# Performance work log

Hardware: AMD Instinct MI355X
Metric: run time of the kernel (lower is better)

The kernel has to match this reference:

```python
import jax, jax.numpy as jnp
import numpy as np

Q_MAX = 127.0  # int8 symmetric quant range


def setup_inputs() -> dict:
    key = jax.random.key(0)
    kx, kw, ks = jax.random.split(key, 3)
    M, K, N = 16384, 4096, 4096
    x = jax.random.normal(kx, (M, K), dtype=jnp.float32)
    # int8 weight values in [-127, 127]
    weight = jax.random.randint(kw, (N, K), -127, 128, dtype=jnp.int32).astype(jnp.int8)
    # per-output-row dequant scale, small positive values as a real quantizer would produce
    weight_scale = jax.random.uniform(ks, (N, 1), dtype=jnp.float32, minval=1e-3, maxval=1e-2)
    return {"x": x, "weight": weight, "weight_scale": weight_scale}


def reference(x, weight, weight_scale):
    # --- per-token dynamic activation quantization (get_hip_quant(per_Token)) ---
    amax = jnp.max(jnp.abs(x), axis=-1, keepdims=True)            # [M,1]
    x_scale = amax / Q_MAX                                        # [M,1]
    x_q = jnp.clip(jnp.round(x / jnp.maximum(x_scale, 1e-8)), -Q_MAX, Q_MAX)  # int8 values, kept fp32
    # --- gemm_a8w8: int8xint8 GEMM with fused dequant (row scale_a * col scale_b) ---
    acc = jnp.einsum('mk,nk->mn', x_q, weight.astype(jnp.float32),
                     preferred_element_type=jnp.float32)          # [M,N] int accumulation in fp32
    y = acc * x_scale * weight_scale.T                            # fused dequant scales
    return y  # fp32 stand-in for otype=bf16 output
```

## Files before the change

### kernel.cpp

```cpp
#include <hip/hip_runtime.h>
#include <stdint.h>

#define M_DIM 16384
#define N_DIM 4096
#define K_DIM 4096

#define BM 256
#define BN 256
#define BK 128
#define NT (K_DIM / BK)

typedef int i32x4 __attribute__((ext_vector_type(4)));

__device__ __forceinline__ void async16(const uint8_t* g, uint8_t* l) {
    __builtin_amdgcn_global_load_lds(
        (const __attribute__((address_space(1))) void*)g,
        (__attribute__((address_space(3))) void*)l,
        16, 0, 0);
}

__global__ __launch_bounds__(256) void pack_w_kernel(const int* __restrict__ w32,
                                                     uint32_t* __restrict__ w8,
                                                     int n4) {
    int i = blockIdx.x * 256 + threadIdx.x;
    if (i < n4) {
        const int4 v = reinterpret_cast<const int4*>(w32)[i];
        uint32_t p = (uint32_t)(v.x & 255) | ((uint32_t)(v.y & 255) << 8) |
                     ((uint32_t)(v.z & 255) << 16) | ((uint32_t)(v.w & 255) << 24);
        w8[i] = p;
    }
}

__global__ __launch_bounds__(256) void quant_kernel(const float* __restrict__ x,
                                                    uint32_t* __restrict__ xq,
                                                    float* __restrict__ xscale) {
    const int m = blockIdx.x;
    const int t = threadIdx.x;
    const float4* row = reinterpret_cast<const float4*>(x + (size_t)m * K_DIM);
    float4 v[4];
    float amax = 0.0f;
#pragma unroll
    for (int i = 0; i < 4; ++i) {
        v[i] = row[t + i * 256];
        amax = fmaxf(amax, fmaxf(fmaxf(fabsf(v[i].x), fabsf(v[i].y)),
                                 fmaxf(fabsf(v[i].z), fabsf(v[i].w))));
    }
#pragma unroll
    for (int off = 32; off > 0; off >>= 1) amax = fmaxf(amax, __shfl_xor(amax, off));
    __shared__ float smax[4];
    if ((t & 63) == 0) smax[t >> 6] = amax;
    __syncthreads();
    amax = fmaxf(fmaxf(smax[0], smax[1]), fmaxf(smax[2], smax[3]));
    const float scale = amax / 127.0f;
    const float s = fmaxf(scale, 1e-8f);
    if (t == 0) xscale[m] = scale;
    uint32_t* orow = xq + (size_t)m * (K_DIM / 4);
#pragma unroll
    for (int i = 0; i < 4; ++i) {
        int q0 = __float2int_rn(v[i].x / s);
        int q1 = __float2int_rn(v[i].y / s);
        int q2 = __float2int_rn(v[i].z / s);
        int q3 = __float2int_rn(v[i].w / s);
        q0 = max(-127, min(127, q0));
        q1 = max(-127, min(127, q1));
        q2 = max(-127, min(127, q2));
        q3 = max(-127, min(127, q3));
        uint32_t p = (uint32_t)(q0 & 255) | ((uint32_t)(q1 & 255) << 8) |
                     ((uint32_t)(q2 & 255) << 16) | ((uint32_t)(q3 & 255) << 24);
        orow[t + i * 256] = p;
    }
}

__global__ __launch_bounds__(512, 2) void gemm_kernel(
    const uint8_t* __restrict__ Aq, const float* __restrict__ ascale,
    const uint8_t* __restrict__ Bq, const float* __restrict__ wscale,
    float* __restrict__ out) {
    __shared__ uint8_t lds[4 * BM * BK];
    uint8_t* ldsA0 = lds;
    uint8_t* ldsA1 = lds + BM * BK;
    uint8_t* ldsB0 = lds + 2 * BM * BK;
    uint8_t* ldsB1 = lds + 3 * BM * BK;

    const int tid = threadIdx.x;
    const int lane = tid & 63;
    const int w = tid >> 6;
    const int wr = w >> 2;
    const int wc = w & 3;
    const int lr = lane & 15;
    const int lg = lane >> 4;

    const int bid = blockIdx.x;
    const int swz = (bid & 7) * (1024 / 8) + (bid >> 3);
    const size_t row0 = (size_t)(swz >> 4) * BM;
    const size_t col0 = (size_t)(swz & 15) * BN;
    const uint8_t* Ab = Aq + row0 * K_DIM;
    const uint8_t* Bb = Bq + col0 * K_DIM;

    i32x4 acc[8][4];
#pragma unroll
    for (int i = 0; i < 8; ++i)
#pragma unroll
        for (int j = 0; j < 4; ++j) acc[i][j] = (i32x4){0, 0, 0, 0};

#define STAGE_P(BASE, DST, KT)                                                   \
    do {                                                                         \
        _Pragma("unroll") for (int it_ = 0; it_ < 4; ++it_) {                    \
            const int idx_ = it_ * 512 + tid;                                    \
            const int m_ = idx_ >> 3, p_ = idx_ & 7;                             \
            async16((BASE) + (size_t)m_ * K_DIM + (KT) * BK +                    \
                        ((p_ ^ (m_ & 7)) << 4),                                  \
                    (DST) + (it_ * 512 + w * 64) * 16);                          \
        }                                                                        \
    } while (0)

#define READ_K(BUFA, BUFB, KK, F)                                                \
    do {                                                                         \
        _Pragma("unroll") for (int q_ = 0; q_ < 8; ++q_) {                       \
            const int r_ = wr * 128 + q_ * 16 + lr;                              \
            const int u_ = (KK) * 4 + lg;                                        \
            afk[F][q_] = *reinterpret_cast<const i32x4*>(                        \
                (BUFA) + r_ * BK + ((u_ ^ (r_ & 7)) << 4));                      \
        }                                                                        \
        _Pragma("unroll") for (int p_ = 0; p_ < 4; ++p_) {                       \
            const int r_ = wc * 64 + p_ * 16 + lr;                               \
            const int u_ = (KK) * 4 + lg;                                        \
            bfk[F][p_] = *reinterpret_cast<const i32x4*>(                        \
                (BUFB) + r_ * BK + ((u_ ^ (r_ & 7)) << 4));                      \
        }                                                                        \
    } while (0)

#define CLUSTER(F)                                                               \
    do {                                                                         \
        __builtin_amdgcn_s_setprio(1);                                           \
        _Pragma("unroll") for (int q_ = 0; q_ < 8; ++q_)                         \
        _Pragma("unroll") for (int p_ = 0; p_ < 4; ++p_)                         \
            acc[q_][p_] = __builtin_amdgcn_mfma_i32_16x16x64_i8(                 \
                afk[F][q_], bfk[F][p_], acc[q_][p_], 0, 0, 0);                   \
        __builtin_amdgcn_s_setprio(0);                                           \
    } while (0)

#define BAR __builtin_amdgcn_s_barrier()
#define VMCNT(N) asm volatile("s_waitcnt vmcnt(" #N ")" ::: "memory")
#define LGKM0                                              \
    do {                                                   \
        asm volatile("s_waitcnt lgkmcnt(0)" ::: "memory"); \
        __builtin_amdgcn_sched_barrier(0);                 \
    } while (0)

    i32x4 afk[2][8], bfk[2][4];

    STAGE_P(Ab, ldsA0, 0);
    STAGE_P(Bb, ldsB0, 0);
    STAGE_P(Ab, ldsA1, 1);
    VMCNT(4);
    BAR;
    READ_K(ldsA0, ldsB0, 0, 0);

#pragma unroll 1
    for (int it2 = 0; it2 < NT / 2; ++it2) {
        const int T = 2 * it2;
        const int Tp2 = (T + 2 < NT) ? T + 2 : NT - 1;
        const int Tp3 = (T + 3 < NT) ? T + 3 : NT - 1;

        LGKM0;
        STAGE_P(Bb, ldsB1, T + 1);
        READ_K(ldsA0, ldsB0, 1, 1);
        CLUSTER(0);
        LGKM0;
        VMCNT(0);
        BAR;
        STAGE_P(Ab, ldsA0, Tp2);
        READ_K(ldsA1, ldsB1, 0, 0);
        CLUSTER(1);

        LGKM0;
        STAGE_P(Bb, ldsB0, Tp2);
        READ_K(ldsA1, ldsB1, 1, 1);
        CLUSTER(0);
        LGKM0;
        VMCNT(0);
        BAR;
        STAGE_P(Ab, ldsA1, Tp3);
        READ_K(ldsA0, ldsB0, 0, 0);
        CLUSTER(1);
    }

    const float* asp = ascale + row0 + wr * 128;
    const float* wsp = wscale + col0 + wc * 64;
    float wsv[4];
#pragma unroll
    for (int nf = 0; nf < 4; ++nf) wsv[nf] = wsp[nf * 16 + lr];
    float* outBase = out + (row0 + wr * 128) * (size_t)N_DIM + col0 + wc * 64;
#pragma unroll
    for (int mf = 0; mf < 8; ++mf) {
#pragma unroll
        for (int j = 0; j < 4; ++j) {
            const int r = mf * 16 + lg * 4 + j;
            const float av = asp[r];
            float* orow = outBase + (size_t)r * N_DIM;
#pragma unroll
            for (int nf = 0; nf < 4; ++nf) {
                orow[nf * 16 + lr] = (float)acc[mf][nf][j] * av * wsv[nf];
            }
        }
    }
#undef STAGE_P
#undef READ_K
#undef CLUSTER
#undef BAR
#undef VMCNT
#undef LGKM0
}

extern "C" void kernel_launch(void* const* d_in, const int* in_sizes, int n_in,
                              void* d_out, int out_size, void* d_ws, size_t ws_size,
                              hipStream_t stream) {
    const float* x = (const float*)d_in[0];
    const int* w32 = (const int*)d_in[1];
    const float* wscale = (const float*)d_in[2];
    float* out = (float*)d_out;

    uint8_t* ws = (uint8_t*)d_ws;
    uint32_t* xq = (uint32_t*)ws;
    float* xscale = (float*)(ws + (size_t)M_DIM * K_DIM);
    uint8_t* wq = ws + (size_t)M_DIM * K_DIM + (size_t)M_DIM * 4;

    pack_w_kernel<<<dim3((N_DIM * K_DIM / 4 + 255) / 256), 256, 0, stream>>>(
        w32, (uint32_t*)wq, N_DIM * K_DIM / 4);
    quant_kernel<<<dim3(M_DIM), 256, 0, stream>>>(x, xq, xscale);
    gemm_kernel<<<dim3((M_DIM / BM) * (N_DIM / BN)), 512, 0, stream>>>(
        (const uint8_t*)xq, xscale, wq, wscale, out);
}
```

Baseline: 348.1 us.

## Load B fragments directly from global into registers, halve LDS footprint

Removes B tiles from LDS staging and has each wave load its B fragments straight from global memory into registers, which halves the shared-memory footprint to only the A double buffer. It also swaps the block swizzle to iterate rows fastest within a column group so B panels stay hot in cache. The aim is less LDS traffic and capacity pressure, possibly allowing better occupancy. The cost is redundant B global loads across the two wave rows and exposed global latency on the B path, which the pipeline must hide.

```diff
diff --git a/kernel.cpp b/kernel.cpp
--- a/kernel.cpp
+++ b/kernel.cpp
@@ -75,11 +75,9 @@
     const uint8_t* __restrict__ Aq, const float* __restrict__ ascale,
     const uint8_t* __restrict__ Bq, const float* __restrict__ wscale,
     float* __restrict__ out) {
-    __shared__ uint8_t lds[4 * BM * BK];
+    __shared__ uint8_t lds[2 * BM * BK];
     uint8_t* ldsA0 = lds;
     uint8_t* ldsA1 = lds + BM * BK;
-    uint8_t* ldsB0 = lds + 2 * BM * BK;
-    uint8_t* ldsB1 = lds + 3 * BM * BK;
 
     const int tid = threadIdx.x;
     const int lane = tid & 63;
@@ -91,10 +89,11 @@
 
     const int bid = blockIdx.x;
     const int swz = (bid & 7) * (1024 / 8) + (bid >> 3);
-    const size_t row0 = (size_t)(swz >> 4) * BM;
-    const size_t col0 = (size_t)(swz & 15) * BN;
+    const size_t col0 = (size_t)(swz >> 6) * BN;
+    const size_t row0 = (size_t)(swz & 63) * BM;
     const uint8_t* Ab = Aq + row0 * K_DIM;
-    const uint8_t* Bb = Bq + col0 * K_DIM;
+
+    const uint8_t* bRow = Bq + (col0 + wc * 64 + lr) * (size_t)K_DIM + lg * 16;
 
     i32x4 acc[8][4];
 #pragma unroll
@@ -102,40 +101,41 @@
 #pragma unroll
         for (int j = 0; j < 4; ++j) acc[i][j] = (i32x4){0, 0, 0, 0};
 
-#define STAGE_P(BASE, DST, KT)                                                   \
+#define STAGE_P(DST, KT)                                                         \
     do {                                                                         \
         _Pragma("unroll") for (int it_ = 0; it_ < 4; ++it_) {                    \
             const int idx_ = it_ * 512 + tid;                                    \
             const int m_ = idx_ >> 3, p_ = idx_ & 7;                             \
-            async16((BASE) + (size_t)m_ * K_DIM + (KT) * BK +                    \
-                        ((p_ ^ (m_ & 7)) << 4),                                  \
+            async16(Ab + (size_t)m_ * K_DIM + (KT) * BK + ((p_ ^ (m_ & 7)) << 4),\
                     (DST) + (it_ * 512 + w * 64) * 16);                          \
         }                                                                        \
     } while (0)
 
-#define READ_K(BUFA, BUFB, KK, F)                                                \
+#define READ_AK(BUF, KK)                                                         \
     do {                                                                         \
         _Pragma("unroll") for (int q_ = 0; q_ < 8; ++q_) {                       \
             const int r_ = wr * 128 + q_ * 16 + lr;                              \
             const int u_ = (KK) * 4 + lg;                                        \
-            afk[F][q_] = *reinterpret_cast<const i32x4*>(                        \
-                (BUFA) + r_ * BK + ((u_ ^ (r_ & 7)) << 4));                      \
+            afk[KK][q_] = *reinterpret_cast<const i32x4*>(                       \
+                (BUF) + r_ * BK + ((u_ ^ (r_ & 7)) << 4));                       \
         }                                                                        \
+    } while (0)
+
+#define LOADB(KK, KT)                                                            \
+    do {                                                                         \
         _Pragma("unroll") for (int p_ = 0; p_ < 4; ++p_) {                       \
-            const int r_ = wc * 64 + p_ * 16 + lr;                               \
-            const int u_ = (KK) * 4 + lg;                                        \
-            bfk[F][p_] = *reinterpret_cast<const i32x4*>(                        \
-                (BUFB) + r_ * BK + ((u_ ^ (r_ & 7)) << 4));                      \
+            bfk[KK][p_] = *reinterpret_cast<const i32x4*>(                       \
+                bRow + (size_t)p_ * 16 * K_DIM + (KT) * BK + (KK) * 64);         \
         }                                                                        \
     } while (0)
 
-#define CLUSTER(F)                                                               \
+#define CLUSTER(KK)                                                              \
     do {                                                                         \
         __builtin_amdgcn_s_setprio(1);                                           \
         _Pragma("unroll") for (int q_ = 0; q_ < 8; ++q_)                         \
         _Pragma("unroll") for (int p_ = 0; p_ < 4; ++p_)                         \
             acc[q_][p_] = __builtin_amdgcn_mfma_i32_16x16x64_i8(                 \
-                afk[F][q_], bfk[F][p_], acc[q_][p_], 0, 0, 0);                   \
+                afk[KK][q_], bfk[KK][p_], acc[q_][p_], 0, 0, 0);                 \
         __builtin_amdgcn_s_setprio(0);                                           \
     } while (0)
 
@@ -147,42 +147,41 @@
         __builtin_amdgcn_sched_barrier(0);                 \
     } while (0)
 
+#define TILE_ONE(CUR, NXT, TB, TA2)                                              \
+    do {                                                                         \
+        LGKM0;                                                                   \
+        READ_AK(CUR, 1);                                                         \
+        CLUSTER(0);                                                              \
+        LOADB(0, TB);                                                            \
+        LGKM0;                                                                   \
+        VMCNT(8);                                                                \
+        BAR;                                                                     \
+        STAGE_P(CUR, TA2);                                                       \
+        READ_AK(NXT, 0);                                                         \
+        CLUSTER(1);                                                              \
+        LOADB(1, TB);                                                            \
+    } while (0)
+
     i32x4 afk[2][8], bfk[2][4];
 
-    STAGE_P(Ab, ldsA0, 0);
-    STAGE_P(Bb, ldsB0, 0);
-    STAGE_P(Ab, ldsA1, 1);
-    VMCNT(4);
+    STAGE_P(ldsA0, 0);
+    STAGE_P(ldsA1, 1);
+    LOADB(0, 0);
+    LOADB(1, 0);
+    VMCNT(0);
     BAR;
-    READ_K(ldsA0, ldsB0, 0, 0);
+    READ_AK(ldsA0, 0);
 
 #pragma unroll 1
     for (int it2 = 0; it2 < NT / 2; ++it2) {
         const int T = 2 * it2;
-        const int Tp2 = (T + 2 < NT) ? T + 2 : NT - 1;
-        const int Tp3 = (T + 3 < NT) ? T + 3 : NT - 1;
-
-        LGKM0;
-        STAGE_P(Bb, ldsB1, T + 1);
-        READ_K(ldsA0, ldsB0, 1, 1);
-        CLUSTER(0);
-        LGKM0;
-        VMCNT(0);
-        BAR;
-        STAGE_P(Ab, ldsA0, Tp2);
-        READ_K(ldsA1, ldsB1, 0, 0);
-        CLUSTER(1);
-
-        LGKM0;
-        STAGE_P(Bb, ldsB0, Tp2);
-        READ_K(ldsA1, ldsB1, 1, 1);
-        CLUSTER(0);
-        LGKM0;
-        VMCNT(0);
-        BAR;
-        STAGE_P(Ab, ldsA1, Tp3);
-        READ_K(ldsA0, ldsB0, 0, 0);
-        CLUSTER(1);
+        const int Tb1 = (T + 1 < NT) ? T + 1 : NT - 1;
+        const int Ta2 = (T + 2 < NT) ? T + 2 : NT - 1;
+        const int Tb2 = Ta2;
+        const int Ta3 = (T + 3 < NT) ? T + 3 : NT - 1;
+
+        TILE_ONE(ldsA0, ldsA1, Tb1, Ta2);
+        TILE_ONE(ldsA1, ldsA0, Tb2, Ta3);
     }
 
     const float* asp = ascale + row0 + wr * 128;
@@ -205,8 +204,10 @@
         }
     }
 #undef STAGE_P
-#undef READ_K
+#undef READ_AK
+#undef LOADB
 #undef CLUSTER
+#undef TILE_ONE
 #undef BAR
 #undef VMCNT
 #undef LGKM0
```

Result: slower. 435.7 us (+25.2%).
